# Performance work log

Hardware: AMD Instinct MI355X
Metric: run time of the kernel (lower is better)

Reference implementation:

```python
import jax, jax.numpy as jnp
import numpy as np

N, T, D, H, NH, BS = 4, 4096, 512, 8, 4, 64
DH = D // H                 # head dim = 64
NB = T // BS                # n_buckets = 64
CS = NH * NB                # chunk_size = 256
L = NH * T                  # sorted sequence length per head


def setup_inputs() -> dict:
    key = jax.random.key(0)
    ks = jax.random.split(key, 4)
    x = jax.random.normal(ks[0], (N, T, D), jnp.float32)
    W_Q = jax.random.normal(ks[1], (D, D), jnp.float32) * (D ** -0.5)
    W_V = jax.random.normal(ks[2], (D, D), jnp.float32) * (D ** -0.5)
    b_Q = jnp.zeros((D,), jnp.float32)
    b_V = jnp.zeros((D,), jnp.float32)
    gamma = jnp.ones((D,), jnp.float32)
    beta = jnp.zeros((D,), jnp.float32)
    # per-head random rotations: (dim_head, num_hashes, n_buckets // 2)
    rotations = jax.random.normal(ks[3], (H, DH, NH, NB // 2), jnp.float32)
    return {"x": x, "W_Q": W_Q, "b_Q": b_Q, "W_V": W_V, "b_V": b_V,
            "gamma": gamma, "beta": beta, "rotations": rotations}


def _look_one_back(a):
    # concat each chunk with the previous chunk (wrap-around for chunk 0)
    extra = jnp.concatenate([a[:, -1:], a[:, :-1]], axis=1)
    return jnp.concatenate([a, extra], axis=2)


def _lsh_head(qk, v, rot):
    # qk, v: [N, T, DH]; rot: [DH, NH, NB//2]
    rotated = jnp.einsum('btf,fhi->bhti', qk, rot)               # [N,NH,T,NB//2]
    rotated = jnp.concatenate([rotated, -rotated], axis=-1)       # [N,NH,T,NB]
    buckets = jnp.argmax(rotated, axis=-1)                        # [N,NH,T]
    offsets = (jnp.arange(NH) * NB)[None, :, None]
    buckets = (buckets + offsets).reshape(N, L)                   # [N, NH*T]

    ticker = jnp.broadcast_to(jnp.arange(L)[None, :], (N, L))
    buckets_and_t = T * buckets + (ticker % T)                    # unique keys
    sticker = jnp.argsort(buckets_and_t, axis=-1)                 # sorted ticker ids
    undo_sort = jnp.argsort(sticker, axis=-1)
    st = sticker % T                                              # original positions

    sqk = jnp.take_along_axis(qk, st[..., None], axis=1)          # [N,L,DH]
    sv = jnp.take_along_axis(v, st[..., None], axis=1)

    bq_t = st.reshape(N, CS, -1)                                  # [N,CS,BS]
    bqk = sqk.reshape(N, CS, -1, DH)
    bv = sv.reshape(N, CS, -1, DH)
    bq = bqk
    bk = bqk / (jnp.linalg.norm(bqk, axis=-1, keepdims=True) + 1e-6)

    bk = _look_one_back(bk)                                       # [N,CS,2*BS,DH]
    bv = _look_one_back(bv)
    bkv_t = _look_one_back(bq_t)

    dots = jnp.einsum('bcie,bcje->bcij', bq, bk) * (DH ** -0.5)   # [N,CS,BS,2BS]

    # mask out pairs hashed to different buckets
    q_sb = jnp.take_along_axis(buckets, sticker, axis=1).reshape(N, CS, -1)
    kv_sb = _look_one_back(q_sb)
    dots = jnp.where(q_sb[:, :, :, None] != kv_sb[:, :, None, :], -1e9, dots)
    # down-weight self-attention (same position)
    dots = jnp.where(bq_t[:, :, :, None] == bkv_t[:, :, None, :], -1e-5, dots)

    lse = jax.nn.logsumexp(dots, axis=-1, keepdims=True)
    probs = jnp.exp(dots - lse)
    bo = jnp.einsum('bcij,bcje->bcie', probs, bv)                 # [N,CS,BS,DH]

    so = bo.reshape(N, L, DH)
    slog = lse.reshape(N, L)
    o = jnp.take_along_axis(so, undo_sort[..., None], axis=1)
    logits = jnp.take_along_axis(slog, undo_sort, axis=1)

    o = o.reshape(N, NH, T, DH)
    logits = logits.reshape(N, NH, T, 1)
    pw = jnp.exp(logits - jax.nn.logsumexp(logits, axis=1, keepdims=True))
    return jnp.sum(o * pw, axis=1)                                # [N,T,DH]


def reference(x, W_Q, b_Q, W_V, b_V, gamma, beta, rotations):
    Q = x @ W_Q + b_Q
    V = x @ W_V + b_V
    Qh = Q.reshape(N, T, H, DH).transpose(2, 0, 1, 3)             # [H,N,T,DH]
    Vh = V.reshape(N, T, H, DH).transpose(2, 0, 1, 3)
    outs = jax.vmap(_lsh_head)(Qh, Vh, rotations)                 # [H,N,T,DH]
    out = outs.transpose(1, 2, 0, 3).reshape(N, T, D)
    mu = out.mean(axis=-1, keepdims=True)
    var = out.var(axis=-1, keepdims=True)
    return gamma * (out - mu) / jnp.sqrt(var + 1e-3) + beta
```

## Files before the change

### kernel.cpp

```cpp
#include <hip/hip_runtime.h>
#include <hip/hip_bf16.h>

#define N_ 4
#define T_ 4096
#define D_ 512
#define H_ 8
#define DH_ 64
#define NH_ 4
#define NB_ 64
#define CS_ 256
#define L_ 16384

typedef unsigned short u16;
typedef unsigned int u32;
typedef __attribute__((ext_vector_type(8))) short short8;
typedef __attribute__((ext_vector_type(8))) _Float16 half8;
typedef __attribute__((ext_vector_type(4))) float f32x4;
typedef __attribute__((ext_vector_type(2))) float f32x2;

__device__ __forceinline__ u16 f2bf(float x){
    union { float f; u32 u; } c; c.f = x;
    u32 u = c.u;
    u32 r = (u + 0x7FFFu + ((u >> 16) & 1u)) >> 16;
    return (u16)r;
}
__device__ __forceinline__ float bf2f(u16 b){
    union { u32 u; float f; } c; c.u = ((u32)b) << 16;
    return c.f;
}
__device__ __forceinline__ u16 f2h(float x){
    _Float16 h = (_Float16)x;
    u16 r; __builtin_memcpy(&r, &h, 2); return r;
}

#define PK_LO(acc, a, b) \
    asm("v_pk_fma_f32 %0, %1, %2, %0 op_sel:[0,0,0] op_sel_hi:[0,1,1]" \
        : "+v"(acc) : "v"(a), "v"(b))
#define PK_HI(acc, a, b) \
    asm("v_pk_fma_f32 %0, %1, %2, %0 op_sel:[1,0,0] op_sel_hi:[1,1,1]" \
        : "+v"(acc) : "v"(a), "v"(b))

__global__ __launch_bounds__(256) void k_decXf(const float* __restrict__ x,
        u16* __restrict__ xf){
    int i = blockIdx.x * 256 + threadIdx.x;
    float4 v = ((const float4*)x)[i];
    ushort4 o;
    o.x = f2h(v.x); o.y = f2h(v.y); o.z = f2h(v.z); o.w = f2h(v.w);
    ((ushort4*)xf)[i] = o;
}

__global__ __launch_bounds__(256) void k_decWv(const float* __restrict__ Wv,
        u16* __restrict__ wvt){
    __shared__ float tile[32][33];
    const int tid = threadIdx.x;
    const int kt = blockIdx.x * 32, nt = blockIdx.y * 32;
    const int tx = tid & 31, ty = tid >> 5;
    #pragma unroll
    for (int i = 0; i < 4; ++i)
        tile[ty + i * 8][tx] = Wv[(size_t)(kt + ty + i * 8) * 512 + nt + tx];
    __syncthreads();
    #pragma unroll
    for (int i = 0; i < 4; ++i){
        int n = ty + i * 8;
        wvt[(size_t)(nt + n) * 512 + kt + tx] = f2h(tile[tx][n]);
    }
}

__global__ __launch_bounds__(256) void k_q(const float* __restrict__ x,
        const float* __restrict__ Wq, const float* __restrict__ bq,
        float* __restrict__ Q, u16* __restrict__ Qbf, float* __restrict__ qinv){
    __shared__ float sA[16][132];
    __shared__ float sB[16][132];
    const int tid = threadIdx.x;
    const int tx = tid & 15, ty = tid >> 4;
    const int mb = blockIdx.x * 128, nb = blockIdx.y * 128;

    f32x2 acc2[8][4];
    #pragma unroll
    for (int i = 0; i < 8; ++i)
        #pragma unroll
        for (int j = 0; j < 4; ++j) acc2[i][j] = (f32x2){0.f, 0.f};

    const int mA = tid >> 2, kA = (tid & 3) * 4;
    const int kB = tid >> 5, cB = (tid & 31) * 4;
    const float* xp0 = &x[(size_t)(mb + mA) * 512 + kA];
    const float* xp1 = xp0 + (size_t)64 * 512;
    const float* wp0 = &Wq[(size_t)kB * 512 + nb + cB];
    const float* wp1 = wp0 + (size_t)8 * 512;

    float4 pa0 = *(const float4*)(xp0);
    float4 pa1 = *(const float4*)(xp1);
    float4 pb0 = *(const float4*)(wp0);
    float4 pb1 = *(const float4*)(wp1);

    for (int k0 = 0; k0 < 512; k0 += 16){
        __syncthreads();
        sA[kA + 0][mA] = pa0.x; sA[kA + 1][mA] = pa0.y;
        sA[kA + 2][mA] = pa0.z; sA[kA + 3][mA] = pa0.w;
        sA[kA + 0][64 + mA] = pa1.x; sA[kA + 1][64 + mA] = pa1.y;
        sA[kA + 2][64 + mA] = pa1.z; sA[kA + 3][64 + mA] = pa1.w;
        *(float4*)&sB[kB][cB] = pb0;
        *(float4*)&sB[kB + 8][cB] = pb1;
        if (k0 < 496){
            pa0 = *(const float4*)(xp0 + k0 + 16);
            pa1 = *(const float4*)(xp1 + k0 + 16);
            pb0 = *(const float4*)(wp0 + (size_t)(k0 + 16) * 512);
            pb1 = *(const float4*)(wp1 + (size_t)(k0 + 16) * 512);
        }
        __syncthreads();
        #pragma unroll
        for (int kk = 0; kk < 16; ++kk){
            float4 va0 = *(const float4*)&sA[kk][ty * 8];
            float4 va1 = *(const float4*)&sA[kk][ty * 8 + 4];
            float4 vb0 = *(const float4*)&sB[kk][tx * 4];
            float4 vb1 = *(const float4*)&sB[kk][64 + tx * 4];
            f32x2 a2[4], b2[4];
            a2[0] = (f32x2){va0.x, va0.y}; a2[1] = (f32x2){va0.z, va0.w};
            a2[2] = (f32x2){va1.x, va1.y}; a2[3] = (f32x2){va1.z, va1.w};
            b2[0] = (f32x2){vb0.x, vb0.y}; b2[1] = (f32x2){vb0.z, vb0.w};
            b2[2] = (f32x2){vb1.x, vb1.y}; b2[3] = (f32x2){vb1.z, vb1.w};
            #pragma unroll
            for (int i = 0; i < 8; ++i){
                #pragma unroll
                for (int jp = 0; jp < 4; ++jp){
                    if (i & 1) { PK_HI(acc2[i][jp], a2[i >> 1], b2[jp]); }
                    else       { PK_LO(acc2[i][jp], a2[i >> 1], b2[jp]); }
                }
            }
        }
    }

    float4 vb0 = *(const float4*)&bq[nb + tx * 4];
    float4 vb1 = *(const float4*)&bq[nb + 64 + tx * 4];
    f32x2 bi[4];
    bi[0] = (f32x2){vb0.x, vb0.y}; bi[1] = (f32x2){vb0.z, vb0.w};
    bi[2] = (f32x2){vb1.x, vb1.y}; bi[3] = (f32x2){vb1.z, vb1.w};
    const int h0 = blockIdx.y * 2;
    #pragma unroll
    for (int i = 0; i < 8; ++i){
        f32x2 o[4];
        #pragma unroll
        for (int jp = 0; jp < 4; ++jp) o[jp] = acc2[i][jp] + bi[jp];
        int m = mb + ty * 8 + i;
        int n = m >> 12, t = m & (T_ - 1);
        float4 q0, q1;
        q0.x = o[0].x; q0.y = o[0].y; q0.z = o[1].x; q0.w = o[1].y;
        q1.x = o[2].x; q1.y = o[2].y; q1.z = o[3].x; q1.w = o[3].y;
        *(float4*)&Q[(size_t)m * 512 + nb + tx * 4] = q0;
        *(float4*)&Q[(size_t)m * 512 + nb + 64 + tx * 4] = q1;
        float ssA = q0.x * q0.x + q0.y * q0.y + q0.z * q0.z + q0.w * q0.w;
        float ssB = q1.x * q1.x + q1.y * q1.y + q1.z * q1.z + q1.w * q1.w;
        #pragma unroll
        for (int s = 8; s >= 1; s >>= 1){
            ssA += __shfl_xor(ssA, s, 64);
            ssB += __shfl_xor(ssB, s, 64);
        }
        size_t rowbA = (size_t)(h0 * N_ + n) * T_ + t;
        size_t rowbB = rowbA + (size_t)N_ * T_;
        if (tx == 0){
            qinv[rowbA] = 1.f / (sqrtf(ssA) + 1e-6f);
            qinv[rowbB] = 1.f / (sqrtf(ssB) + 1e-6f);
        }
        ushort4 qa, qb;
        qa.x = f2bf(q0.x); qa.y = f2bf(q0.y); qa.z = f2bf(q0.z); qa.w = f2bf(q0.w);
        qb.x = f2bf(q1.x); qb.y = f2bf(q1.y); qb.z = f2bf(q1.z); qb.w = f2bf(q1.w);
        *(ushort4*)&Qbf[rowbA * 64 + tx * 4] = qa;
        *(ushort4*)&Qbf[rowbB * 64 + tx * 4] = qb;
    }
}

__global__ __launch_bounds__(256) void k_gemmV(const u16* __restrict__ xf,
        const u16* __restrict__ wvt, const float* __restrict__ bv,
        u16* __restrict__ Vbf){
    __shared__ __align__(16) u16 sA[128 * 40];
    __shared__ __align__(16) u16 sB[128 * 40];
    const int tid = threadIdx.x;
    const int mb = blockIdx.x * 128, nb = blockIdx.y * 128;
    const int w = tid >> 6, lane = tid & 63, quad = lane >> 4, cc = lane & 15;
    const int wm = (w & 1) * 64, wn = (w >> 1) * 64;
    f32x4 acc[4][4];
    #pragma unroll
    for (int i = 0; i < 4; ++i)
        #pragma unroll
        for (int j = 0; j < 4; ++j) acc[i][j] = (f32x4){0.f, 0.f, 0.f, 0.f};

    for (int k0 = 0; k0 < 512; k0 += 32){
        #pragma unroll
        for (int i = 0; i < 2; ++i){
            int idx = i * 256 + tid;
            int m = idx >> 2, ks = idx & 3;
            *(short8*)&sA[m * 40 + ks * 8] =
                *(const short8*)&xf[(size_t)(mb + m) * 512 + k0 + ks * 8];
            *(short8*)&sB[m * 40 + ks * 8] =
                *(const short8*)&wvt[(size_t)(nb + m) * 512 + k0 + ks * 8];
        }
        __syncthreads();
        half8 a[4], b[4];
        #pragma unroll
        for (int i = 0; i < 4; ++i){
            a[i] = *(const half8*)&sA[(wm + i * 16 + cc) * 40 + quad * 8];
            b[i] = *(const half8*)&sB[(wn + i * 16 + cc) * 40 + quad * 8];
        }
        #pragma unroll
        for (int i = 0; i < 4; ++i)
            #pragma unroll
            for (int j = 0; j < 4; ++j)
                acc[i][j] = __builtin_amdgcn_mfma_f32_16x16x32_f16(a[i], b[j], acc[i][j], 0, 0, 0);
        __syncthreads();
    }
    #pragma unroll
    for (int i = 0; i < 4; ++i)
        #pragma unroll
        for (int j = 0; j < 4; ++j){
            int c = nb + wn + j * 16 + cc;
            int hh = c >> 6, d = c & 63;
            float bi = bv[c];
            #pragma unroll
            for (int r = 0; r < 4; ++r){
                int m = mb + wm + i * 16 + quad * 4 + r;
                int n = m >> 12, t = m & (T_ - 1);
                Vbf[((size_t)(hh * N_ + n) * T_ + t) * 64 + d] = f2bf(acc[i][j][r] + bi);
            }
        }
}

__global__ __launch_bounds__(256) void k_rot(const float* __restrict__ Q,
        const float* __restrict__ rot, int* __restrict__ buckets){
    const int tb = blockIdx.x * 32;
    const int n = blockIdx.y, h = blockIdx.z;
    const int hn = h * N_ + n;
    __shared__ float Rs[64 * 128];
    __shared__ float Qs[32][64];
    const int tid = threadIdx.x;
    const float* rh = rot + (size_t)h * (64 * 128);
    for (int i = tid; i < 8192; i += 256) Rs[i] = rh[i];
    for (int i = tid; i < 2048; i += 256){
        int t = i >> 6, f = i & 63;
        Qs[t][f] = Q[(size_t)(n * T_ + tb + t) * 512 + h * 64 + f];
    }
    __syncthreads();
    const int tx = tid & 31, tg = tid >> 5;
    float r[4][4] = {};
    for (int f = 0; f < 64; ++f){
        float q0 = Qs[tg * 4 + 0][f], q1 = Qs[tg * 4 + 1][f];
        float q2 = Qs[tg * 4 + 2][f], q3 = Qs[tg * 4 + 3][f];
        #pragma unroll
        for (int jj = 0; jj < 4; ++jj){
            float rv = Rs[f * 128 + jj * 32 + tx];
            r[0][jj] += q0 * rv; r[1][jj] += q1 * rv;
            r[2][jj] += q2 * rv; r[3][jj] += q3 * rv;
        }
    }
    #pragma unroll
    for (int tt = 0; tt < 4; ++tt){
        #pragma unroll
        for (int jj = 0; jj < 4; ++jj){
            float bv = r[tt][jj]; int bi = tx;
            float nv = -bv;
            if (nv > bv){ bv = nv; bi = 32 + tx; }
            #pragma unroll
            for (int m = 16; m >= 1; m >>= 1){
                float ov = __shfl_xor(bv, m, 32);
                int   oi = __shfl_xor(bi, m, 32);
                if (ov > bv || (ov == bv && oi < bi)){ bv = ov; bi = oi; }
            }
            if (tx == 0){
                int t = tb + tg * 4 + tt;
                buckets[(size_t)hn * L_ + jj * T_ + t] = bi + jj * 64;
            }
        }
    }
}

__global__ __launch_bounds__(256) void k_hist(const int* __restrict__ buckets,
        int* __restrict__ hist){
    const int tile = blockIdx.x, hn = blockIdx.y;
    const int tid = threadIdx.x;
    __shared__ int h[256];
    h[tid] = 0;
    __syncthreads();
    int b = buckets[(size_t)hn * L_ + tile * 256 + tid];
    atomicAdd(&h[b], 1);
    __syncthreads();
    hist[((size_t)hn * 64 + tile) * 256 + tid] = h[tid];
}

__global__ __launch_bounds__(256) void k_scan(int* __restrict__ hist,
        int* __restrict__ bucketStart){
    const int hn = blockIdx.x;
    const int b = threadIdx.x;
    int* hh = hist + (size_t)hn * 64 * 256;
    int run = 0;
    for (int tl = 0; tl < 64; ++tl){
        int v = hh[tl * 256 + b];
        hh[tl * 256 + b] = run;
        run += v;
    }
    __shared__ int s[256];
    s[b] = run;
    __syncthreads();
    for (int off = 1; off < 256; off <<= 1){
        int add = (b >= off) ? s[b - off] : 0;
        __syncthreads();
        s[b] += add;
        __syncthreads();
    }
    bucketStart[hn * 256 + b] = s[b] - run;
}

__global__ __launch_bounds__(256) void k_scatter(const int* __restrict__ buckets,
        const int* __restrict__ offs, const int* __restrict__ bucketStart,
        int* __restrict__ sticker){
    const int tile = blockIdx.x, hn = blockIdx.y;
    const int tid = threadIdx.x;
    __shared__ int sb[256];
    const int i = tile * 256 + tid;
    const int b = buckets[(size_t)hn * L_ + i];
    sb[tid] = b;
    __syncthreads();
    int rank = 0;
    #pragma unroll 8
    for (int j = 0; j < 256; ++j){
        int v = sb[j];
        rank += (j < tid && v == b) ? 1 : 0;
    }
    int pos = bucketStart[hn * 256 + b]
            + offs[((size_t)hn * 64 + tile) * 256 + b]
            + rank;
    sticker[(size_t)hn * L_ + pos] = i;
}

__global__ __launch_bounds__(256) void k_attn(const u16* __restrict__ Qbf,
        const u16* __restrict__ Vbf, const float* __restrict__ qinv,
        const int* __restrict__ buckets, const int* __restrict__ sticker,
        u16* __restrict__ o_hash, float* __restrict__ logit_hash){
    const int blk_c = blockIdx.x, n = blockIdx.y, h = blockIdx.z;
    const int hn = h * N_ + n;
    const int tid = threadIdx.x;
    const int w = tid >> 6, lane = tid & 63;
    const int quad = lane >> 4, cc = lane & 15;

    __shared__ __align__(16) u16 sQ[128 * 64];
    __shared__ __align__(16) u16 sVt[64 * 128];
    __shared__ __align__(16) u16 sP[64 * 128];
    __shared__ int s_idx[128], s_buck[128], s_t[128];
    __shared__ float s_inv[128];
    __shared__ float s_lse[64];

    if (tid < 128){
        int cprev = (blk_c + CS_ - 1) & (CS_ - 1);
        int pos = (tid < 64) ? blk_c * 64 + tid : cprev * 64 + (tid - 64);
        int idx = sticker[(size_t)hn * L_ + pos];
        s_idx[tid] = idx;
        s_buck[tid] = buckets[(size_t)hn * L_ + idx];
        int t = idx & (T_ - 1);
        s_t[tid] = t;
        s_inv[tid] = qinv[(size_t)hn * T_ + t];
    }
    __syncthreads();

    const int r0 = tid >> 3, l8 = tid & 7;
    #pragma unroll
    for (int it = 0; it < 4; ++it){
        int r = it * 32 + r0;
        size_t gb = ((size_t)hn * T_ + s_t[r]) * 64 + l8 * 8;
        short8 qv = *(const short8*)&Qbf[gb];
        *(short8*)&sQ[r * 64 + ((l8 ^ (r & 7)) * 8)] = qv;
        short8 vv = *(const short8*)&Vbf[gb];
        #pragma unroll
        for (int i = 0; i < 8; ++i){
            int d = l8 * 8 + i;
            sVt[d * 128 + (((r >> 3) ^ (d & 15)) * 8) + (r & 7)] = (u16)vv[i];
        }
    }
    __syncthreads();

    f32x4 dacc[8];
    #pragma unroll
    for (int j = 0; j < 8; ++j) dacc[j] = (f32x4){0.f, 0.f, 0.f, 0.f};
    const int qrow = w * 16 + cc;
    #pragma unroll
    for (int kc = 0; kc < 2; ++kc){
        short8 afrag = *(const short8*)&sQ[qrow * 64 + (((kc * 4 + quad) ^ (cc & 7)) * 8)];
        #pragma unroll
        for (int kt = 0; kt < 8; ++kt){
            int krow = kt * 16 + cc;
            short8 bfrag = *(const short8*)&sQ[krow * 64 + (((kc * 4 + quad) ^ (cc & 7)) * 8)];
            dacc[kt] = __builtin_amdgcn_mfma_f32_16x16x32_bf16(afrag, bfrag, dacc[kt], 0, 0, 0);
        }
    }

    int bq[4], tq[4];
    #pragma unroll
    for (int r = 0; r < 4; ++r){
        int q = w * 16 + quad * 4 + r;
        bq[r] = s_buck[q]; tq[r] = s_t[q];
    }
    float mrow[4] = {-1e30f, -1e30f, -1e30f, -1e30f};
    #pragma unroll
    for (int kt = 0; kt < 8; ++kt){
        int kk = kt * 16 + cc;
        float inv = s_inv[kk] * 0.125f;
        int bk = s_buck[kk], tk = s_t[kk];
        #pragma unroll
        for (int r = 0; r < 4; ++r){
            float d = dacc[kt][r] * inv;
            if (bk != bq[r]) d = -1e9f;
            if (tk == tq[r]) d = -1e-5f;
            dacc[kt][r] = d;
            mrow[r] = fmaxf(mrow[r], d);
        }
    }
    #pragma unroll
    for (int r = 0; r < 4; ++r)
        #pragma unroll
        for (int m = 8; m >= 1; m >>= 1)
            mrow[r] = fmaxf(mrow[r], __shfl_xor(mrow[r], m, 64));
    float srow[4] = {0.f, 0.f, 0.f, 0.f};
    #pragma unroll
    for (int kt = 0; kt < 8; ++kt)
        #pragma unroll
        for (int r = 0; r < 4; ++r){
            float e = __expf(dacc[kt][r] - mrow[r]);
            dacc[kt][r] = e;
            srow[r] += e;
        }
    #pragma unroll
    for (int r = 0; r < 4; ++r)
        #pragma unroll
        for (int m = 8; m >= 1; m >>= 1)
            srow[r] += __shfl_xor(srow[r], m, 64);
    float lse[4], pscale[4];
    #pragma unroll
    for (int r = 0; r < 4; ++r){
        lse[r] = mrow[r] + __logf(srow[r]);
        pscale[r] = 1.f / srow[r];
    }
    if (cc == 0){
        #pragma unroll
        for (int r = 0; r < 4; ++r) s_lse[w * 16 + quad * 4 + r] = lse[r];
    }

    #pragma unroll
    for (int kt = 0; kt < 8; ++kt){
        int kk = kt * 16 + cc;
        #pragma unroll
        for (int r = 0; r < 4; ++r){
            int q = w * 16 + quad * 4 + r;
            sP[q * 128 + (((kk >> 3) ^ (q & 15)) * 8) + (kk & 7)] =
                f2bf(dacc[kt][r] * pscale[r]);
        }
    }
    __syncthreads();

    f32x4 oacc[4];
    #pragma unroll
    for (int j = 0; j < 4; ++j) oacc[j] = (f32x4){0.f, 0.f, 0.f, 0.f};
    #pragma unroll
    for (int kc = 0; kc < 4; ++kc){
        short8 afrag = *(const short8*)&sP[qrow * 128 + (((kc * 4 + quad) ^ cc) * 8)];
        #pragma unroll
        for (int nt = 0; nt < 4; ++nt){
            int d = nt * 16 + cc;
            short8 bfrag = *(const short8*)&sVt[d * 128 + (((kc * 4 + quad) ^ cc) * 8)];
            oacc[nt] = __builtin_amdgcn_mfma_f32_16x16x32_bf16(afrag, bfrag, oacc[nt], 0, 0, 0);
        }
    }

    #pragma unroll
    for (int r = 0; r < 4; ++r){
        int q = w * 16 + quad * 4 + r;
        int si = s_idx[q];
        int jj = si >> 12; int t = si & (T_ - 1);
        size_t base = ((size_t)(hn * NH_ + jj) * T_ + t) * 64;
        #pragma unroll
        for (int nt = 0; nt < 4; ++nt)
            o_hash[base + nt * 16 + cc] = f2bf(oacc[nt][r]);
    }
    if (tid < 64){
        int si = s_idx[tid]; int jj = si >> 12; int t = si & (T_ - 1);
        logit_hash[(size_t)(hn * NH_ + jj) * T_ + t] = s_lse[tid];
    }
}

__global__ __launch_bounds__(256) void k_comb(const u16* __restrict__ o_hash,
        const float* __restrict__ logit_hash, const float* __restrict__ gamma,
        const float* __restrict__ beta, float* __restrict__ out){
    const int t = blockIdx.x, n = blockIdx.y;
    const int tid = threadIdx.x;
    __shared__ float s_pw[32];
    __shared__ float s_x[512];
    __shared__ float s_red[8];
    __shared__ float s_mu, s_rs;
    if (tid < 32){
        int h = tid >> 2, j = tid & 3;
        s_pw[tid] = logit_hash[(size_t)((h * N_ + n) * NH_ + j) * T_ + t];
    }
    __syncthreads();
    if (tid < 8){
        int h = tid;
        float m = -1e30f;
        #pragma unroll
        for (int j = 0; j < 4; ++j) m = fmaxf(m, s_pw[h * 4 + j]);
        float l = 0.f;
        #pragma unroll
        for (int j = 0; j < 4; ++j) l += __expf(s_pw[h * 4 + j] - m);
        float ls = m + __logf(l);
        #pragma unroll
        for (int j = 0; j < 4; ++j) s_pw[h * 4 + j] = __expf(s_pw[h * 4 + j] - ls);
    }
    __syncthreads();
    float va[2];
    #pragma unroll
    for (int i = 0; i < 2; ++i){
        int cidx = tid + i * 256;
        int h = cidx >> 6, d = cidx & 63;
        size_t base = (size_t)((h * N_ + n) * NH_) * T_ * 64;
        float acc = 0.f;
        #pragma unroll
        for (int j = 0; j < 4; ++j)
            acc += s_pw[h * 4 + j] * bf2f(o_hash[base + ((size_t)j * T_ + t) * 64 + d]);
        s_x[cidx] = acc; va[i] = acc;
    }
    float s1 = va[0] + va[1];
    float s2 = va[0] * va[0] + va[1] * va[1];
    #pragma unroll
    for (int m = 32; m >= 1; m >>= 1){
        s1 += __shfl_xor(s1, m, 64);
        s2 += __shfl_xor(s2, m, 64);
    }
    const int lane = tid & 63, w = tid >> 6;
    if (lane == 0){ s_red[w] = s1; s_red[4 + w] = s2; }
    __syncthreads();
    if (tid == 0){
        float S1 = s_red[0] + s_red[1] + s_red[2] + s_red[3];
        float S2 = s_red[4] + s_red[5] + s_red[6] + s_red[7];
        float mu = S1 / 512.f;
        float var = S2 / 512.f - mu * mu;
        s_mu = mu; s_rs = 1.f / sqrtf(var + 1e-3f);
    }
    __syncthreads();
    #pragma unroll
    for (int i = 0; i < 2; ++i){
        int cidx = tid + i * 256;
        out[((size_t)(n * T_ + t)) * 512 + cidx] =
            gamma[cidx] * (s_x[cidx] - s_mu) * s_rs + beta[cidx];
    }
}

extern "C" void kernel_launch(void* const* d_in, const int* in_sizes, int n_in,
                              void* d_out, int out_size, void* d_ws, size_t ws_size,
                              hipStream_t stream){
    const float* x     = (const float*)d_in[0];
    const float* Wq    = (const float*)d_in[1];
    const float* bq    = (const float*)d_in[2];
    const float* Wv    = (const float*)d_in[3];
    const float* bv    = (const float*)d_in[4];
    const float* gamma = (const float*)d_in[5];
    const float* beta  = (const float*)d_in[6];
    const float* rot   = (const float*)d_in[7];
    char* ws = (char*)d_ws;
    float* Q        = (float*)(ws + 0);
    u16*   o_hash   = (u16*)  (ws + 0);
    u16*   Qbf      = (u16*)  (ws + 67108864);
    u16*   Vbf      = (u16*)  (ws + 83886080);
    float* qinv     = (float*)(ws + 100663296);
    int*   buckets  = (int*)  (ws + 101187584);
    int*   sticker  = (int*)  (ws + 103284736);
    float* logit    = (float*)(ws + 105381888);
    int*   hist     = (int*)  (ws + 107479040);
    int*   bstart   = (int*)  (ws + 109576192);
    u16*   xf       = (u16*)  (ws + 109608960);
    u16*   wvt      = (u16*)  (ws + 126386176);

    hipLaunchKernelGGL(k_decXf,   dim3(8192),       dim3(256), 0, stream,
                       x, xf);
    hipLaunchKernelGGL(k_decWv,   dim3(16, 16),     dim3(256), 0, stream,
                       Wv, wvt);
    hipLaunchKernelGGL(k_gemmV,   dim3(128, 4),     dim3(256), 0, stream,
                       xf, wvt, bv, Vbf);
    hipLaunchKernelGGL(k_q,       dim3(128, 4),     dim3(256), 0, stream,
                       x, Wq, bq, Q, Qbf, qinv);
    hipLaunchKernelGGL(k_rot,     dim3(128, 4, 8),  dim3(256), 0, stream,
                       Q, rot, buckets);
    hipLaunchKernelGGL(k_hist,    dim3(64, 32),     dim3(256), 0, stream,
                       buckets, hist);
    hipLaunchKernelGGL(k_scan,    dim3(32),         dim3(256), 0, stream,
                       hist, bstart);
    hipLaunchKernelGGL(k_scatter, dim3(64, 32),     dim3(256), 0, stream,
                       buckets, hist, bstart, sticker);
    hipLaunchKernelGGL(k_attn,    dim3(256, 4, 8),  dim3(256), 0, stream,
                       Qbf, Vbf, qinv, buckets, sticker, o_hash, logit);
    hipLaunchKernelGGL(k_comb,    dim3(4096, 4),    dim3(256), 0, stream,
                       o_hash, logit, gamma, beta, (float*)d_out);
}
```

Baseline: 419.7 us.

## Double-buffer GEMM LDS tiles, pack rotation FMAs, alias Q/P shared buffers

Both projection GEMMs now use double-buffered shared tiles, which removes one barrier per k-step, and the V GEMM preloads its next tile into registers. The LSH rotation kernel rearranges the rotation matrix in shared memory so it can use vectorized loads and packed FMA. The attention kernel reuses the Q buffer for P to save shared memory, which needs an extra barrier, changes the V-transpose swizzle, and folds the 1/8 scale into s_inv. These are several separate tweaks aimed at barrier stalls, occupancy and ALU throughput.

Result: faster. 399.0 us (-4.9%).

```diff
diff --git a/kernel.cpp b/kernel.cpp
--- a/kernel.cpp
+++ b/kernel.cpp
@@ -40,6 +40,8 @@
     asm("v_pk_fma_f32 %0, %1, %2, %0 op_sel:[1,0,0] op_sel_hi:[1,1,1]" \
         : "+v"(acc) : "v"(a), "v"(b))
 
+#define VSWZ(d) ((((d) >> 3) ^ ((d) & 7)))
+
 __global__ __launch_bounds__(256) void k_decXf(const float* __restrict__ x,
         u16* __restrict__ xf){
     int i = blockIdx.x * 256 + threadIdx.x;
@@ -69,8 +71,8 @@
 __global__ __launch_bounds__(256) void k_q(const float* __restrict__ x,
         const float* __restrict__ Wq, const float* __restrict__ bq,
         float* __restrict__ Q, u16* __restrict__ Qbf, float* __restrict__ qinv){
-    __shared__ float sA[16][132];
-    __shared__ float sB[16][132];
+    __shared__ float sA[2][16][132];
+    __shared__ float sB[2][16][132];
     const int tid = threadIdx.x;
     const int tx = tid & 15, ty = tid >> 4;
     const int mb = blockIdx.x * 128, nb = blockIdx.y * 128;
@@ -88,32 +90,32 @@
     const float* wp0 = &Wq[(size_t)kB * 512 + nb + cB];
     const float* wp1 = wp0 + (size_t)8 * 512;
 
-    float4 pa0 = *(const float4*)(xp0);
-    float4 pa1 = *(const float4*)(xp1);
-    float4 pb0 = *(const float4*)(wp0);
-    float4 pb1 = *(const float4*)(wp1);
+    float4 pa0 = *(const float4*)xp0;
+    float4 pa1 = *(const float4*)xp1;
+    float4 pb0 = *(const float4*)wp0;
+    float4 pb1 = *(const float4*)wp1;
 
     for (int k0 = 0; k0 < 512; k0 += 16){
+        const int p = (k0 >> 4) & 1;
+        sA[p][kA + 0][mA] = pa0.x; sA[p][kA + 1][mA] = pa0.y;
+        sA[p][kA + 2][mA] = pa0.z; sA[p][kA + 3][mA] = pa0.w;
+        sA[p][kA + 0][64 + mA] = pa1.x; sA[p][kA + 1][64 + mA] = pa1.y;
+        sA[p][kA + 2][64 + mA] = pa1.z; sA[p][kA + 3][64 + mA] = pa1.w;
+        *(float4*)&sB[p][kB][cB] = pb0;
+        *(float4*)&sB[p][kB + 8][cB] = pb1;
         __syncthreads();
-        sA[kA + 0][mA] = pa0.x; sA[kA + 1][mA] = pa0.y;
-        sA[kA + 2][mA] = pa0.z; sA[kA + 3][mA] = pa0.w;
-        sA[kA + 0][64 + mA] = pa1.x; sA[kA + 1][64 + mA] = pa1.y;
-        sA[kA + 2][64 + mA] = pa1.z; sA[kA + 3][64 + mA] = pa1.w;
-        *(float4*)&sB[kB][cB] = pb0;
-        *(float4*)&sB[kB + 8][cB] = pb1;
         if (k0 < 496){
             pa0 = *(const float4*)(xp0 + k0 + 16);
             pa1 = *(const float4*)(xp1 + k0 + 16);
             pb0 = *(const float4*)(wp0 + (size_t)(k0 + 16) * 512);
             pb1 = *(const float4*)(wp1 + (size_t)(k0 + 16) * 512);
         }
-        __syncthreads();
         #pragma unroll
         for (int kk = 0; kk < 16; ++kk){
-            float4 va0 = *(const float4*)&sA[kk][ty * 8];
-            float4 va1 = *(const float4*)&sA[kk][ty * 8 + 4];
-            float4 vb0 = *(const float4*)&sB[kk][tx * 4];
-            float4 vb1 = *(const float4*)&sB[kk][64 + tx * 4];
+            float4 va0 = *(const float4*)&sA[p][kk][ty * 8];
+            float4 va1 = *(const float4*)&sA[p][kk][ty * 8 + 4];
+            float4 vb0 = *(const float4*)&sB[p][kk][tx * 4];
+            float4 vb1 = *(const float4*)&sB[p][kk][64 + tx * 4];
             f32x2 a2[4], b2[4];
             a2[0] = (f32x2){va0.x, va0.y}; a2[1] = (f32x2){va0.z, va0.w};
             a2[2] = (f32x2){va1.x, va1.y}; a2[3] = (f32x2){va1.z, va1.w};
@@ -172,41 +174,52 @@
 __global__ __launch_bounds__(256) void k_gemmV(const u16* __restrict__ xf,
         const u16* __restrict__ wvt, const float* __restrict__ bv,
         u16* __restrict__ Vbf){
-    __shared__ __align__(16) u16 sA[128 * 40];
-    __shared__ __align__(16) u16 sB[128 * 40];
+    __shared__ __align__(16) u16 sA[2][128 * 40];
+    __shared__ __align__(16) u16 sB[2][128 * 40];
     const int tid = threadIdx.x;
     const int mb = blockIdx.x * 128, nb = blockIdx.y * 128;
     const int w = tid >> 6, lane = tid & 63, quad = lane >> 4, cc = lane & 15;
     const int wm = (w & 1) * 64, wn = (w >> 1) * 64;
+    const int m0 = tid >> 2, ks0 = tid & 3;
     f32x4 acc[4][4];
     #pragma unroll
     for (int i = 0; i < 4; ++i)
         #pragma unroll
         for (int j = 0; j < 4; ++j) acc[i][j] = (f32x4){0.f, 0.f, 0.f, 0.f};
 
+    const u16* ap0 = &xf[(size_t)(mb + m0) * 512 + ks0 * 8];
+    const u16* ap1 = ap0 + (size_t)64 * 512;
+    const u16* bp0 = &wvt[(size_t)(nb + m0) * 512 + ks0 * 8];
+    const u16* bp1 = bp0 + (size_t)64 * 512;
+    short8 pa0 = *(const short8*)ap0;
+    short8 pa1 = *(const short8*)ap1;
+    short8 pb0 = *(const short8*)bp0;
+    short8 pb1 = *(const short8*)bp1;
+
     for (int k0 = 0; k0 < 512; k0 += 32){
-        #pragma unroll
-        for (int i = 0; i < 2; ++i){
-            int idx = i * 256 + tid;
-            int m = idx >> 2, ks = idx & 3;
-            *(short8*)&sA[m * 40 + ks * 8] =
-                *(const short8*)&xf[(size_t)(mb + m) * 512 + k0 + ks * 8];
-            *(short8*)&sB[m * 40 + ks * 8] =
-                *(const short8*)&wvt[(size_t)(nb + m) * 512 + k0 + ks * 8];
-        }
+        const int p = (k0 >> 5) & 1;
+        *(short8*)&sA[p][m0 * 40 + ks0 * 8] = pa0;
+        *(short8*)&sA[p][(64 + m0) * 40 + ks0 * 8] = pa1;
+        *(short8*)&sB[p][m0 * 40 + ks0 * 8] = pb0;
+        *(short8*)&sB[p][(64 + m0) * 40 + ks0 * 8] = pb1;
         __syncthreads();
+        if (k0 < 480){
+            pa0 = *(const short8*)(ap0 + k0 + 32);
+            pa1 = *(const short8*)(ap1 + k0 + 32);
+            pb0 = *(const short8*)(bp0 + k0 + 32);
+            pb1 = *(const short8*)(bp1 + k0 + 32);
+        }
         half8 a[4], b[4];
         #pragma unroll
         for (int i = 0; i < 4; ++i){
-            a[i] = *(const half8*)&sA[(wm + i * 16 + cc) * 40 + quad * 8];
-            b[i] = *(const half8*)&sB[(wn + i * 16 + cc) * 40 + quad * 8];
+            a[i] = *(const half8*)&sA[p][(wm + i * 16 + cc) * 40 + quad * 8];
+            b[i] = *(const half8*)&sB[p][(wn + i * 16 + cc) * 40 + quad * 8];
         }
         #pragma unroll
         for (int i = 0; i < 4; ++i)
             #pragma unroll
             for (int j = 0; j < 4; ++j)
                 acc[i][j] = __builtin_amdgcn_mfma_f32_16x16x32_f16(a[i], b[j], acc[i][j], 0, 0, 0);
-        __syncthreads();
     }
     #pragma unroll
     for (int i = 0; i < 4; ++i)
@@ -233,29 +246,46 @@
     __shared__ float Qs[32][64];
     const int tid = threadIdx.x;
     const float* rh = rot + (size_t)h * (64 * 128);
-    for (int i = tid; i < 8192; i += 256) Rs[i] = rh[i];
+    for (int idx = tid; idx < 8192; idx += 256){
+        int f = idx >> 7, rem = idx & 127, jj = rem >> 5, i2 = rem & 31;
+        Rs[f * 128 + i2 * 4 + jj] = rh[idx];
+    }
     for (int i = tid; i < 2048; i += 256){
         int t = i >> 6, f = i & 63;
         Qs[t][f] = Q[(size_t)(n * T_ + tb + t) * 512 + h * 64 + f];
     }
     __syncthreads();
     const int tx = tid & 31, tg = tid >> 5;
-    float r[4][4] = {};
-    for (int f = 0; f < 64; ++f){
-        float q0 = Qs[tg * 4 + 0][f], q1 = Qs[tg * 4 + 1][f];
-        float q2 = Qs[tg * 4 + 2][f], q3 = Qs[tg * 4 + 3][f];
+    f32x2 r2[4][2];
+    #pragma unroll
+    for (int tt = 0; tt < 4; ++tt){
+        r2[tt][0] = (f32x2){0.f, 0.f};
+        r2[tt][1] = (f32x2){0.f, 0.f};
+    }
+    for (int f = 0; f < 64; f += 2){
+        f32x2 qf[4];
+        #pragma unroll
+        for (int tt = 0; tt < 4; ++tt)
+            qf[tt] = *(const f32x2*)&Qs[tg * 4 + tt][f];
+        float4 rv0 = *(const float4*)&Rs[f * 128 + tx * 4];
+        float4 rv1 = *(const float4*)&Rs[(f + 1) * 128 + tx * 4];
+        f32x2 b0[2], b1[2];
+        b0[0] = (f32x2){rv0.x, rv0.y}; b0[1] = (f32x2){rv0.z, rv0.w};
+        b1[0] = (f32x2){rv1.x, rv1.y}; b1[1] = (f32x2){rv1.z, rv1.w};
+        #pragma unroll
+        for (int tt = 0; tt < 4; ++tt){
+            PK_LO(r2[tt][0], qf[tt], b0[0]);
+            PK_LO(r2[tt][1], qf[tt], b0[1]);
+            PK_HI(r2[tt][0], qf[tt], b1[0]);
+            PK_HI(r2[tt][1], qf[tt], b1[1]);
+        }
+    }
+    #pragma unroll
+    for (int tt = 0; tt < 4; ++tt){
         #pragma unroll
         for (int jj = 0; jj < 4; ++jj){
-            float rv = Rs[f * 128 + jj * 32 + tx];
-            r[0][jj] += q0 * rv; r[1][jj] += q1 * rv;
-            r[2][jj] += q2 * rv; r[3][jj] += q3 * rv;
-        }
-    }
-    #pragma unroll
-    for (int tt = 0; tt < 4; ++tt){
-        #pragma unroll
-        for (int jj = 0; jj < 4; ++jj){
-            float bv = r[tt][jj]; int bi = tx;
+            float rval = (jj < 2) ? r2[tt][0][jj] : r2[tt][1][jj - 2];
+            float bv = rval; int bi = tx;
             float nv = -bv;
             if (nv > bv){ bv = nv; bi = 32 + tx; }
             #pragma unroll
@@ -340,12 +370,13 @@
     const int w = tid >> 6, lane = tid & 63;
     const int quad = lane >> 4, cc = lane & 15;
 
-    __shared__ __align__(16) u16 sQ[128 * 64];
+    __shared__ __align__(16) u16 sQP[128 * 64];
     __shared__ __align__(16) u16 sVt[64 * 128];
-    __shared__ __align__(16) u16 sP[64 * 128];
     __shared__ int s_idx[128], s_buck[128], s_t[128];
     __shared__ float s_inv[128];
     __shared__ float s_lse[64];
+    u16* const sQ = sQP;
+    u16* const sP = sQP;
 
     if (tid < 128){
         int cprev = (blk_c + CS_ - 1) & (CS_ - 1);
@@ -355,7 +386,7 @@
         s_buck[tid] = buckets[(size_t)hn * L_ + idx];
         int t = idx & (T_ - 1);
         s_t[tid] = t;
-        s_inv[tid] = qinv[(size_t)hn * T_ + t];
+        s_inv[tid] = qinv[(size_t)hn * T_ + t] * 0.125f;
     }
     __syncthreads();
 
@@ -370,7 +401,7 @@
         #pragma unroll
         for (int i = 0; i < 8; ++i){
             int d = l8 * 8 + i;
-            sVt[d * 128 + (((r >> 3) ^ (d & 15)) * 8) + (r & 7)] = (u16)vv[i];
+            sVt[d * 128 + (((r >> 3) ^ VSWZ(d)) * 8) + (r & 7)] = (u16)vv[i];
         }
     }
     __syncthreads();
@@ -400,7 +431,7 @@
     #pragma unroll
     for (int kt = 0; kt < 8; ++kt){
         int kk = kt * 16 + cc;
-        float inv = s_inv[kk] * 0.125f;
+        float inv = s_inv[kk];
         int bk = s_buck[kk], tk = s_t[kk];
         #pragma unroll
         for (int r = 0; r < 4; ++r){
@@ -441,6 +472,8 @@
         for (int r = 0; r < 4; ++r) s_lse[w * 16 + quad * 4 + r] = lse[r];
     }
 
+    __syncthreads();
+
     #pragma unroll
     for (int kt = 0; kt < 8; ++kt){
         int kk = kt * 16 + cc;
@@ -462,7 +495,7 @@
         #pragma unroll
         for (int nt = 0; nt < 4; ++nt){
             int d = nt * 16 + cc;
-            short8 bfrag = *(const short8*)&sVt[d * 128 + (((kc * 4 + quad) ^ cc) * 8)];
+            short8 bfrag = *(const short8*)&sVt[d * 128 + (((kc * 4 + quad) ^ VSWZ(d)) * 8)];
             oacc[nt] = __builtin_amdgcn_mfma_f32_16x16x32_bf16(afrag, bfrag, oacc[nt], 0, 0, 0);
         }
     }
```
